# Performance work log

Hardware: AMD Instinct MI355X
Metric: run time of the kernel (lower is better)

## Reference

```python
import jax, jax.numpy as jnp
import numpy as np

N_NODES = 50000
N_EDGES = 300000
D = 256          # in_dim = out_dim (residual)
DE = 256         # edge relation dim
K = 2            # num_kgs
H = 4            # heads
L = 2            # layers
DH = D // H


def _routed_linear(x, W, b, idx):
    # x:[E,din], W:[K,din,dout], b:[K,dout], idx:[E] in [0,K)
    # Compute all K branches (K is tiny) then select per edge.
    outs = jnp.einsum('ed,kdo->keo', x, W) + b[:, None, :]
    return outs[idx, jnp.arange(idx.shape[0])]


def _layernorm(x, g, b):
    mu = jnp.mean(x, axis=-1, keepdims=True)
    var = jnp.mean(jnp.square(x - mu), axis=-1, keepdims=True)
    return (x - mu) * jax.lax.rsqrt(var + 1e-5) * g + b


def _mga_layer(h, src, dst, kg_src, kg_dst, beta, rel,
               ln_g, ln_b, Wt, bt, Wq, bq, Wk, bk):
    N = h.shape[0]
    E = src.shape[0]
    residual = h
    hn = _layernorm(h, ln_g, ln_b)
    x_j = hn[src]                       # [E,D] gathered source feats
    x_i = hn[dst]                       # [E,D] gathered target feats
    # per-edge KG-routed transfer of concatenated (x_j, relation emb)
    xj_t = jax.nn.gelu(_routed_linear(jnp.concatenate([x_j, rel], axis=1), Wt, bt, kg_src),
                       approximate=False)
    q = _routed_linear(x_i, Wq, bq, kg_dst).reshape(E, H, DH)
    k = _routed_linear(xj_t, Wk, bk, kg_src).reshape(E, H, DH)
    # per-edge multi-head dot product, scaled by edge_beta_r then 1/sqrt(dh)
    att = jnp.sum(q * k, axis=-1) * beta[:, None] / jnp.sqrt(jnp.asarray(DH, h.dtype))  # [E,H]
    # scatter-softmax over incoming edges of each target node
    m = jax.ops.segment_max(att, dst, num_segments=N)          # [N,H]
    e = jnp.exp(att - m[dst])
    denom = jax.ops.segment_sum(e, dst, num_segments=N)        # [N,H]
    a = e / (denom[dst] + 1e-16)                                # [E,H]
    msg = (a[:, :, None] * xj_t.reshape(E, H, DH)).reshape(E, D)
    aggr = jax.ops.segment_sum(msg, dst, num_segments=N)        # [N,D]
    return residual + jax.nn.gelu(aggr, approximate=False)


def setup_inputs() -> dict:
    key = jax.random.key(0)
    ks = jax.random.split(key, 10)
    x = jax.random.normal(ks[0], (N_NODES, D), dtype=jnp.float32)
    edge_index = jax.random.randint(ks[1], (2, N_EDGES), 0, N_NODES, dtype=jnp.int32)
    edge_kg_index = jax.random.randint(ks[2], (2, N_EDGES), 0, K, dtype=jnp.int32)
    edge_beta_r = jax.random.uniform(ks[3], (N_EDGES,), dtype=jnp.float32)
    edge_rel_emb = jax.random.normal(ks[4], (N_EDGES, DE), dtype=jnp.float32)
    return {
        'x': x,
        'edge_index': edge_index,
        'edge_kg_index': edge_kg_index,
        'edge_beta_r': edge_beta_r,
        'edge_rel_emb': edge_rel_emb,
        'ln_g': jnp.ones((L, D), jnp.float32),
        'ln_b': jnp.zeros((L, D), jnp.float32),
        'Wt': jax.random.normal(ks[5], (L, K, D + DE, D), jnp.float32) / np.sqrt(D + DE),
        'bt': jnp.zeros((L, K, D), jnp.float32),
        'Wq': jax.random.normal(ks[6], (L, K, D, D), jnp.float32) / np.sqrt(D),
        'bq': jnp.zeros((L, K, D), jnp.float32),
        'Wk': jax.random.normal(ks[7], (L, K, D, D), jnp.float32) / np.sqrt(D),
        'bk': jnp.zeros((L, K, D), jnp.float32),
    }


def reference(x, edge_index, edge_kg_index, edge_beta_r, edge_rel_emb,
              ln_g, ln_b, Wt, bt, Wq, bq, Wk, bk):
    src, dst = edge_index[0], edge_index[1]          # j (source), i (target)
    kg_src, kg_dst = edge_kg_index[0], edge_kg_index[1]
    h = x  # dropout is identity in eval mode
    for l in range(L):
        h = _mga_layer(h, src, dst, kg_src, kg_dst, edge_beta_r, edge_rel_emb,
                       ln_g[l], ln_b[l], Wt[l], bt[l], Wq[l], bq[l], Wk[l], bk[l])
    return h
```

## Files before the change

### kernel.cpp

```cpp
#include <hip/hip_runtime.h>
#include <hip/hip_bf16.h>

#define NN 50000
#define NE 300000
#define DD 256
#define NCHUNK 293

typedef __hip_bfloat16 bf16;
typedef __attribute__((ext_vector_type(8))) short bf16x8;
typedef __attribute__((ext_vector_type(4))) float f32x4;

__device__ __forceinline__ float bf2f(bf16 v) { return __bfloat162float(v); }
__device__ __forceinline__ unsigned short f2b(float v) {
    bf16 t = __float2bfloat16(v);
    return *reinterpret_cast<unsigned short*>(&t);
}
__device__ __forceinline__ float b2f_bits(unsigned short u) {
    return __uint_as_float(((unsigned)u) << 16);
}
__device__ __forceinline__ float gelu_f(float v) {
    float v2 = v * v;
    float z  = v * fmaf(v2, 0.044715f, 1.0f) * 0.7978845608f;
    float e  = __expf(2.0f * z);
    float th = 1.0f - 2.0f / (e + 1.0f);
    return 0.5f * v * (1.0f + th);
}
__device__ __forceinline__ void gl2lds16(const uint4* g, uint4* l) {
    __builtin_amdgcn_global_load_lds(
        (const __attribute__((address_space(1))) void*)g,
        (__attribute__((address_space(3))) void*)l, 16, 0, 0);
}

__global__ void part_count(const int* __restrict__ kg, int* __restrict__ bcnt) {
    int base = blockIdx.x * 1024;
    __shared__ int wc[4];
    int t = threadIdx.x, wave = t >> 6, lane = t & 63;
    int cnt = 0;
    #pragma unroll
    for (int s = 0; s < 4; ++s) {
        int j = base + s * 256 + t;
        int is0 = (j < NE && kg[j] == 0) ? 1 : 0;
        unsigned long long m = __ballot(is0);
        if (lane == 0) cnt += __popcll(m);
    }
    if (lane == 0) wc[wave] = cnt;
    __syncthreads();
    if (t == 0) bcnt[blockIdx.x] = wc[0] + wc[1] + wc[2] + wc[3];
}

__global__ void part_scan(const int* __restrict__ bcnt, int* __restrict__ bofs,
                          int* __restrict__ meta, int n) {
    if (threadIdx.x == 0 && blockIdx.x == 0) {
        int run = 0;
        for (int i = 0; i < n; ++i) { bofs[i] = run; run += bcnt[i]; }
        meta[0] = run;
    }
}

__global__ void part_scatter(const int* __restrict__ kg, const int* __restrict__ bofs,
                             const int* __restrict__ meta, int* __restrict__ perm) {
    int base = blockIdx.x * 1024;
    int c0 = meta[0];
    __shared__ int wz[4];
    int t = threadIdx.x, wave = t >> 6, lane = t & 63;
    int zrun = bofs[blockIdx.x];
    for (int s = 0; s < 4; ++s) {
        int j = base + s * 256 + t;
        int valid = j < NE;
        int is0 = (valid && kg[j] == 0) ? 1 : 0;
        unsigned long long m = __ballot(is0);
        int zb = __popcll(m & ((1ull << lane) - 1ull));
        if (lane == 0) wz[wave] = __popcll(m);
        __syncthreads();
        int wbefore = 0;
        for (int w = 0; w < wave; ++w) wbefore += wz[w];
        int zeros_before = zrun + wbefore + zb;
        if (valid) {
            int pos = is0 ? zeros_before : (c0 + (j - zeros_before));
            perm[pos] = j;
        }
        int stepz = wz[0] + wz[1] + wz[2] + wz[3];
        __syncthreads();
        zrun += stepz;
    }
}

__global__ void deg_hist(const int* __restrict__ dst, int* __restrict__ deg) {
    int i = blockIdx.x * blockDim.x + threadIdx.x;
    if (i < NE) atomicAdd(&deg[dst[i]], 1);
}

__global__ __launch_bounds__(1024) void scan_nodes(const int* __restrict__ deg,
                                                   int* __restrict__ ofs) {
    __shared__ int pex[1025];
    int t = threadIdx.x;
    const int C = (NN + 1023) / 1024;
    int base = t * C;
    int s = 0;
    for (int j = 0; j < C; ++j) { int idx = base + j; if (idx < NN) s += deg[idx]; }
    pex[t + 1] = s;
    __syncthreads();
    if (t == 0) {
        pex[0] = 0;
        for (int i = 1; i <= 1024; ++i) pex[i] += pex[i - 1];
    }
    __syncthreads();
    int run = pex[t];
    for (int j = 0; j < C; ++j) {
        int idx = base + j;
        if (idx < NN) { ofs[idx] = run; run += deg[idx]; }
    }
    if (t == 1023) ofs[NN] = pex[1024];
}

__global__ void copy_int(const int* __restrict__ a, int* __restrict__ b, int n) {
    int i = blockIdx.x * blockDim.x + threadIdx.x;
    if (i < n) b[i] = a[i];
}

__global__ void csr_fill(const int* __restrict__ dst, int* __restrict__ cur,
                         int* __restrict__ eid) {
    int i = blockIdx.x * blockDim.x + threadIdx.x;
    if (i < NE) {
        int p = atomicAdd(&cur[dst[i]], 1);
        eid[p] = i;
    }
}

__global__ void f2b_vec_kernel(const float* __restrict__ in, ushort* __restrict__ out, long n4) {
    long i0 = (long)blockIdx.x * blockDim.x + threadIdx.x;
    long stride = (long)gridDim.x * blockDim.x;
    for (long i = i0; i < n4; i += stride) {
        float4 v = ((const float4*)in)[i];
        ushort4 o;
        o.x = f2b(v.x); o.y = f2b(v.y); o.z = f2b(v.z); o.w = f2b(v.w);
        ((ushort4*)out)[i] = o;
    }
}

__global__ void transpose_w_kernel(const float* __restrict__ in, ushort* __restrict__ out,
                                   int shift, long total) {
    long i0 = (long)blockIdx.x * blockDim.x + threadIdx.x;
    long stride = (long)gridDim.x * blockDim.x;
    long dmask = ((long)1 << shift) - 1;
    for (long i = i0; i < total; i += stride) {
        long d = i & dmask;
        long rest = i >> shift;
        long o = rest & 255;
        long s = rest >> 8;
        out[i] = f2b(in[((s << shift) + d) * 256 + o]);
    }
}

__global__ void fill_kernel(float* __restrict__ p, float v, int n) {
    for (int i = blockIdx.x * blockDim.x + threadIdx.x; i < n; i += gridDim.x * blockDim.x)
        p[i] = v;
}

__global__ __launch_bounds__(256) void lnx_kernel(const float* __restrict__ x,
        const float* __restrict__ g, const float* __restrict__ b,
        float* __restrict__ h, bf16* __restrict__ hn) {
    int n = blockIdx.x * 4 + (threadIdx.x >> 6);
    if (n >= NN) return;
    int t = threadIdx.x & 63;
    float4 v = ((const float4*)(x + (size_t)n * DD))[t];
    ((float4*)(h + (size_t)n * DD))[t] = v;
    float s  = v.x + v.y + v.z + v.w;
    float s2 = v.x * v.x + v.y * v.y + v.z * v.z + v.w * v.w;
    #pragma unroll
    for (int off = 32; off; off >>= 1) {
        s  += __shfl_down(s, off);
        s2 += __shfl_down(s2, off);
    }
    s = __shfl(s, 0); s2 = __shfl(s2, 0);
    float mu  = s * (1.f / DD);
    float var = s2 * (1.f / DD) - mu * mu;
    float rs  = rsqrtf(var + 1e-5f);
    float vv[4] = {v.x, v.y, v.z, v.w};
    ushort4 pk;
    unsigned short* pku = (unsigned short*)&pk;
    #pragma unroll
    for (int j = 0; j < 4; ++j) {
        int c = t * 4 + j;
        pku[j] = f2b((vv[j] - mu) * rs * g[c] + b[c]);
    }
    ((ushort4*)(hn + (size_t)n * DD))[t] = pk;
}

__global__ __launch_bounds__(512) void qn_mfma(
        const bf16* __restrict__ hn, const ushort* __restrict__ WqT,
        const float* __restrict__ bq, ushort* __restrict__ qn) {
    __shared__ uint4 xh[64 * 32];
    __shared__ float bqs[2][256];
    int t = threadIdx.x;
    int n0 = blockIdx.x * 64;
    int wave = t >> 6, lane = t & 63;
    if (t < 256) { bqs[0][t] = bq[t]; bqs[1][t] = bq[256 + t]; }
    const uint4* hn4 = (const uint4*)hn;
    #pragma unroll
    for (int j = 0; j < 4; ++j) {
        int pr = wave * 4 + j;
        int r2 = pr * 2 + (lane >> 5);
        int node = n0 + r2; if (node >= NN) node = NN - 1;
        int s = lane & 31;
        gl2lds16(hn4 + (size_t)node * 32 + (s ^ (r2 & 7)), &xh[pr * 64]);
    }
    __syncthreads();
    int lr = lane & 15, lg = lane >> 4;
    f32x4 acc[2][2][4];
    #pragma unroll
    for (int b = 0; b < 2; ++b)
        #pragma unroll
        for (int m = 0; m < 2; ++m)
            #pragma unroll
            for (int n = 0; n < 4; ++n) acc[b][m][n] = (f32x4){0.f, 0.f, 0.f, 0.f};
    const char* xhb = (const char*)xh;
    const ushort* qr0 = WqT + (size_t)(wave * 32 + lr) * 256 + lg * 8;
    const ushort* qr1 = WqT + (size_t)(wave * 32 + 16 + lr) * 256 + lg * 8;
    #pragma unroll
    for (int kk = 0; kk < 8; ++kk) {
        bf16x8 a00 = *(const bf16x8*)(qr0 + kk * 32);
        bf16x8 a01 = *(const bf16x8*)(qr1 + kk * 32);
        bf16x8 a10 = *(const bf16x8*)(qr0 + 65536 + kk * 32);
        bf16x8 a11 = *(const bf16x8*)(qr1 + 65536 + kk * 32);
        bf16x8 bfr[4];
        #pragma unroll
        for (int n = 0; n < 4; ++n) {
            int r = n * 16 + lr;
            bfr[n] = *(const bf16x8*)(xhb + r * 512 + (((kk * 4 + lg) ^ (r & 7)) << 4));
        }
        #pragma unroll
        for (int n = 0; n < 4; ++n) {
            acc[0][0][n] = __builtin_amdgcn_mfma_f32_16x16x32_bf16(a00, bfr[n], acc[0][0][n], 0, 0, 0);
            acc[0][1][n] = __builtin_amdgcn_mfma_f32_16x16x32_bf16(a01, bfr[n], acc[0][1][n], 0, 0, 0);
            acc[1][0][n] = __builtin_amdgcn_mfma_f32_16x16x32_bf16(a10, bfr[n], acc[1][0][n], 0, 0, 0);
            acc[1][1][n] = __builtin_amdgcn_mfma_f32_16x16x32_bf16(a11, bfr[n], acc[1][1][n], 0, 0, 0);
        }
    }
    #pragma unroll
    for (int n = 0; n < 4; ++n) {
        int e = n * 16 + lr;
        int node = n0 + e;
        if (node < NN) {
            #pragma unroll
            for (int br = 0; br < 2; ++br)
                #pragma unroll
                for (int m = 0; m < 2; ++m) {
                    int ob = wave * 32 + m * 16 + lg * 4;
                    f32x4 a = acc[br][m][n];
                    ushort4 pk;
                    unsigned short* pu = (unsigned short*)&pk;
                    #pragma unroll
                    for (int r = 0; r < 4; ++r) pu[r] = f2b(a[r] + bqs[br][ob + r]);
                    *(ushort4*)(qn + ((size_t)br * NN + node) * 256 + ob) = pk;
                }
        }
    }
}

template<int RELB>
__global__ __launch_bounds__(512, 4) void transfer_mfma(
        const bf16* __restrict__ hn, const float* __restrict__ rel,
        const ushort* __restrict__ relb,
        const int* __restrict__ src, const int* __restrict__ dst,
        const int* __restrict__ kgd,
        const int* __restrict__ perm, const int* __restrict__ meta,
        const ushort* __restrict__ WtT, const float* __restrict__ bt,
        const ushort* __restrict__ WkT, const float* __restrict__ bk,
        const ushort* __restrict__ qn, const float* __restrict__ beta,
        bf16* __restrict__ xjt, float* __restrict__ att) {
    __shared__ uint4 xh[64 * 32];
    __shared__ float bts[256], bks[256];
    __shared__ float patt[8][64];
    __shared__ int sge[64], ssrc[64], sdst[64], sgd[64], sval[64];
    int t = threadIdx.x;
    int c0 = meta[0];
    int tiles0 = (c0 + 63) >> 6;
    int tiles1 = (NE - c0 + 63) >> 6;
    int bid = blockIdx.x;
    if (bid >= tiles0 + tiles1) return;
    int kgt, start, end;
    if (bid < tiles0) { kgt = 0; start = bid * 64; end = c0; }
    else              { kgt = 1; start = c0 + (bid - tiles0) * 64; end = NE; }
    int wave = t >> 6, lane = t & 63;
    if (t < 64) {
        int pos = start + t;
        int v = pos < end;
        int ge = perm[v ? pos : end - 1];
        sge[t] = ge; sval[t] = v; ssrc[t] = src[ge]; sdst[t] = dst[ge]; sgd[t] = kgd[ge];
    } else if (t >= 256) {
        int c = t & 255;
        bts[c] = bt[kgt * 256 + c];
        bks[c] = bk[kgt * 256 + c];
    }
    __syncthreads();
    const uint4* hn4 = (const uint4*)hn;
    #pragma unroll
    for (int j = 0; j < 4; ++j) {
        int pr = wave * 4 + j;
        int r2 = pr * 2 + (lane >> 5);
        int s = lane & 31;
        gl2lds16(hn4 + (size_t)ssrc[r2] * 32 + (s ^ (r2 & 7)), &xh[pr * 64]);
    }
    __syncthreads();
    int lr = lane & 15, lg = lane >> 4;
    ushort4 kv[2][4];
    #pragma unroll
    for (int n = 0; n < 4; ++n) {
        int e = n * 16 + lr;
        size_t qb = ((size_t)sgd[e] * NN + sdst[e]) * 256;
        #pragma unroll
        for (int m = 0; m < 2; ++m) {
            int ob = wave * 32 + m * 16 + lg * 4;
            kv[m][n] = *(const ushort4*)(qn + qb + ob);
        }
    }
    f32x4 acc[2][4];
    #pragma unroll
    for (int m = 0; m < 2; ++m)
        #pragma unroll
        for (int n = 0; n < 4; ++n) acc[m][n] = (f32x4){0.f, 0.f, 0.f, 0.f};
    const char* xhb = (const char*)xh;
    const ushort* wb = WtT + (size_t)kgt * 131072;
    const ushort* wrow0 = wb + (size_t)(wave * 32 + lr) * 512 + lg * 8;
    const ushort* wrow1 = wb + (size_t)(wave * 32 + 16 + lr) * 512 + lg * 8;
    __builtin_amdgcn_s_setprio(1);
    #pragma unroll
    for (int kk = 0; kk < 8; ++kk) {
        bf16x8 a0 = *(const bf16x8*)(wrow0 + kk * 32);
        bf16x8 a1 = *(const bf16x8*)(wrow1 + kk * 32);
        bf16x8 bfr[4];
        #pragma unroll
        for (int n = 0; n < 4; ++n) {
            int r = n * 16 + lr;
            bfr[n] = *(const bf16x8*)(xhb + r * 512 + (((kk * 4 + lg) ^ (r & 7)) << 4));
        }
        #pragma unroll
        for (int m = 0; m < 2; ++m)
            #pragma unroll
            for (int n = 0; n < 4; ++n)
                acc[m][n] = __builtin_amdgcn_mfma_f32_16x16x32_bf16((m ? a1 : a0), bfr[n], acc[m][n], 0, 0, 0);
    }
    __builtin_amdgcn_s_setprio(0);
    __syncthreads();
    if (RELB) {
        const uint4* rb4 = (const uint4*)relb;
        #pragma unroll
        for (int j = 0; j < 4; ++j) {
            int pr = wave * 4 + j;
            int r2 = pr * 2 + (lane >> 5);
            int s = lane & 31;
            gl2lds16(rb4 + (size_t)sge[r2] * 32 + (s ^ (r2 & 7)), &xh[pr * 64]);
        }
    } else {
        #pragma unroll
        for (int i = 0; i < 8; ++i) {
            int r = i * 8 + wave;
            float4 f = ((const float4*)(rel + (size_t)sge[r] * 256))[lane];
            ushort4 o;
            o.x = f2b(f.x); o.y = f2b(f.y); o.z = f2b(f.z); o.w = f2b(f.w);
            int s = lane >> 1;
            char* bp = (char*)&xh[r * 32] + (((s ^ (r & 7)) << 4) | ((lane & 1) << 3));
            *(ushort4*)bp = o;
        }
    }
    __syncthreads();
    __builtin_amdgcn_s_setprio(1);
    #pragma unroll
    for (int kk = 8; kk < 16; ++kk) {
        bf16x8 a0 = *(const bf16x8*)(wrow0 + kk * 32);
        bf16x8 a1 = *(const bf16x8*)(wrow1 + kk * 32);
        int ks = (kk & 7) * 4 + lg;
        bf16x8 bfr[4];
        #pragma unroll
        for (int n = 0; n < 4; ++n) {
            int r = n * 16 + lr;
            bfr[n] = *(const bf16x8*)(xhb + r * 512 + ((ks ^ (r & 7)) << 4));
        }
        #pragma unroll
        for (int m = 0; m < 2; ++m)
            #pragma unroll
            for (int n = 0; n < 4; ++n)
                acc[m][n] = __builtin_amdgcn_mfma_f32_16x16x32_bf16((m ? a1 : a0), bfr[n], acc[m][n], 0, 0, 0);
    }
    __builtin_amdgcn_s_setprio(0);
    __syncthreads();
    char* xob = (char*)xh;
    #pragma unroll
    for (int n = 0; n < 4; ++n) {
        int e = n * 16 + lr;
        #pragma unroll
        for (int m = 0; m < 2; ++m) {
            int ob = wave * 32 + m * 16 + lg * 4;
            f32x4 a = acc[m][n];
            ushort4 pk;
            unsigned short* pu = (unsigned short*)&pk;
            #pragma unroll
            for (int r = 0; r < 4; ++r)
                pu[r] = f2b(gelu_f(a[r] + bts[ob + r]));
            int bofs = ob * 2;
            int slot = ((bofs >> 4) ^ (e & 7));
            *(ushort4*)(xob + e * 512 + slot * 16 + (bofs & 15)) = pk;
        }
    }
    __syncthreads();
    #pragma unroll
    for (int m = 0; m < 2; ++m)
        #pragma unroll
        for (int n = 0; n < 4; ++n) acc[m][n] = (f32x4){0.f, 0.f, 0.f, 0.f};
    const ushort* kbw = WkT + (size_t)kgt * 65536;
    const ushort* kr0 = kbw + (size_t)(wave * 32 + lr) * 256 + lg * 8;
    const ushort* kr1 = kbw + (size_t)(wave * 32 + 16 + lr) * 256 + lg * 8;
    __builtin_amdgcn_s_setprio(1);
    #pragma unroll
    for (int kk = 0; kk < 8; ++kk) {
        bf16x8 a0 = *(const bf16x8*)(kr0 + kk * 32);
        bf16x8 a1 = *(const bf16x8*)(kr1 + kk * 32);
        bf16x8 bfr[4];
        #pragma unroll
        for (int n = 0; n < 4; ++n) {
            int r = n * 16 + lr;
            bfr[n] = *(const bf16x8*)(xob + r * 512 + (((kk * 4 + lg) ^ (r & 7)) << 4));
        }
        #pragma unroll
        for (int n = 0; n < 4; ++n) {
            acc[0][n] = __builtin_amdgcn_mfma_f32_16x16x32_bf16(a0, bfr[n], acc[0][n], 0, 0, 0);
            acc[1][n] = __builtin_amdgcn_mfma_f32_16x16x32_bf16(a1, bfr[n], acc[1][n], 0, 0, 0);
        }
    }
    __builtin_amdgcn_s_setprio(0);
    float p[4];
    #pragma unroll
    for (int n = 0; n < 4; ++n) {
        float s = 0.f;
        #pragma unroll
        for (int m = 0; m < 2; ++m) {
            int ob = wave * 32 + m * 16 + lg * 4;
            ushort4 qv = kv[m][n];
            f32x4 kcv = acc[m][n];
            s = fmaf(b2f_bits(qv.x), kcv[0] + bks[ob + 0], s);
            s = fmaf(b2f_bits(qv.y), kcv[1] + bks[ob + 1], s);
            s = fmaf(b2f_bits(qv.z), kcv[2] + bks[ob + 2], s);
            s = fmaf(b2f_bits(qv.w), kcv[3] + bks[ob + 3], s);
        }
        p[n] = s;
    }
    #pragma unroll
    for (int n = 0; n < 4; ++n) {
        p[n] += __shfl_xor(p[n], 16);
        p[n] += __shfl_xor(p[n], 32);
    }
    if (lane < 16) {
        #pragma unroll
        for (int n = 0; n < 4; ++n) patt[wave][n * 16 + lr] = p[n];
    }
    uint4* xjv = (uint4*)xjt;
    #pragma unroll
    for (int i = 0; i < 4; ++i) {
        int flat = i * 512 + t;
        int r = flat >> 5, c = flat & 31;
        if (sval[r])
            xjv[(size_t)sge[r] * 32 + c] = *(const uint4*)(xob + r * 512 + ((c ^ (r & 7)) << 4));
    }
    __syncthreads();
    if (t < 256) {
        int e = t & 63, h = t >> 6;
        if (sval[e]) {
            int ge = sge[e];
            att[(size_t)ge * 4 + h] = (patt[2 * h][e] + patt[2 * h + 1][e]) * beta[ge] * 0.125f;
        }
    }
}

template<int WRITE_HN>
__global__ __launch_bounds__(256) void aggregate_kernel(
        const float* __restrict__ att, const bf16* __restrict__ xjt,
        const int* __restrict__ eid, const int* __restrict__ ofs,
        float* __restrict__ h, const float* __restrict__ g, const float* __restrict__ b,
        bf16* __restrict__ hn) {
    int node = blockIdx.x * 4 + (threadIdx.x >> 6);
    if (node >= NN) return;
    int lane = threadIdx.x & 63;
    int hh = lane >> 4;
    int beg = ofs[node], end = ofs[node + 1];
    float m = -1e30f;
    for (int i = beg; i < end; ++i)
        m = fmaxf(m, att[(size_t)eid[i] * 4 + hh]);
    float den = 0.f;
    float a0 = 0.f, a1 = 0.f, a2 = 0.f, a3 = 0.f;
    for (int i = beg; i < end; ++i) {
        int e = eid[i];
        float wgt = __expf(att[(size_t)e * 4 + hh] - m);
        den += wgt;
        ushort4 v = *(const ushort4*)((const ushort*)xjt + (size_t)e * 256 + lane * 4);
        a0 = fmaf(wgt, b2f_bits(v.x), a0);
        a1 = fmaf(wgt, b2f_bits(v.y), a1);
        a2 = fmaf(wgt, b2f_bits(v.z), a2);
        a3 = fmaf(wgt, b2f_bits(v.w), a3);
    }
    float inv = 1.f / (den + 1e-16f);
    float4 hv = ((float4*)(h + (size_t)node * 256))[lane];
    hv.x += gelu_f(a0 * inv);
    hv.y += gelu_f(a1 * inv);
    hv.z += gelu_f(a2 * inv);
    hv.w += gelu_f(a3 * inv);
    ((float4*)(h + (size_t)node * 256))[lane] = hv;
    if (WRITE_HN) {
        float s  = hv.x + hv.y + hv.z + hv.w;
        float s2 = hv.x * hv.x + hv.y * hv.y + hv.z * hv.z + hv.w * hv.w;
        #pragma unroll
        for (int off = 32; off; off >>= 1) {
            s  += __shfl_down(s, off);
            s2 += __shfl_down(s2, off);
        }
        s = __shfl(s, 0); s2 = __shfl(s2, 0);
        float mu  = s * (1.f / DD);
        float var = s2 * (1.f / DD) - mu * mu;
        float rs  = rsqrtf(var + 1e-5f);
        float vv[4] = {hv.x, hv.y, hv.z, hv.w};
        ushort4 pk;
        unsigned short* pku = (unsigned short*)&pk;
        #pragma unroll
        for (int j = 0; j < 4; ++j) {
            int c = lane * 4 + j;
            pku[j] = f2b((vv[j] - mu) * rs * g[c] + b[c]);
        }
        ((ushort4*)(hn + (size_t)node * DD))[lane] = pk;
    }
}

extern "C" void kernel_launch(void* const* d_in, const int* in_sizes, int n_in,
                              void* d_out, int out_size, void* d_ws, size_t ws_size,
                              hipStream_t stream) {
    const float* x    = (const float*)d_in[0];
    const int*   ei   = (const int*)d_in[1];
    const int*   ekg  = (const int*)d_in[2];
    const float* beta = (const float*)d_in[3];
    const float* rel  = (const float*)d_in[4];
    const float* ln_g = (const float*)d_in[5];
    const float* ln_b = (const float*)d_in[6];
    const float* Wt   = (const float*)d_in[7];
    const float* bt   = (const float*)d_in[8];
    const float* Wq   = (const float*)d_in[9];
    const float* bq   = (const float*)d_in[10];
    const float* Wk   = (const float*)d_in[11];
    const float* bk   = (const float*)d_in[12];

    float* h = (float*)d_out;

    const int* srcp = ei;
    const int* dstp = ei + NE;
    const int* kgs  = ekg;
    const int* kgd  = ekg + NE;

    char* w = (char*)d_ws;
    float*  att   = (float*)w;  w += (size_t)NE * 4 * 4;
    bf16*   hn    = (bf16*)w;   w += (size_t)NN * DD * 2;
    bf16*   xjt   = (bf16*)w;   w += (size_t)NE * DD * 2;
    ushort* qn    = (ushort*)w; w += (size_t)2 * NN * DD * 2;
    ushort* WtT   = (ushort*)w; w += (size_t)4 * 256 * 512 * 2;
    ushort* WqT   = (ushort*)w; w += (size_t)4 * 256 * 256 * 2;
    ushort* WkT   = (ushort*)w; w += (size_t)4 * 256 * 256 * 2;
    int* perm_src = (int*)w;    w += (size_t)NE * 4;
    int* bcnt0    = (int*)w;    w += NCHUNK * 4;
    int* bofs0    = (int*)w;    w += NCHUNK * 4;
    int* meta0    = (int*)w;    w += 64;
    int* deg      = (int*)w;    w += (size_t)NN * 4;
    int* ofs      = (int*)w;    w += (size_t)(NN + 1) * 4;
    int* cur      = (int*)w;    w += (size_t)NN * 4;
    int* eid      = (int*)w;    w += (size_t)NE * 4;
    size_t used = (size_t)(w - (char*)d_ws);
    ushort* relb = (ushort*)w;
    int use_relb = (ws_size >= used + (size_t)NE * DD * 2) ? 1 : 0;

    part_count<<<NCHUNK, 256, 0, stream>>>(kgs, bcnt0);
    part_scan<<<1, 64, 0, stream>>>(bcnt0, bofs0, meta0, NCHUNK);
    part_scatter<<<NCHUNK, 256, 0, stream>>>(kgs, bofs0, meta0, perm_src);

    fill_kernel<<<64, 256, 0, stream>>>((float*)deg, 0.f, NN);
    deg_hist<<<(NE + 255) / 256, 256, 0, stream>>>(dstp, deg);
    scan_nodes<<<1, 1024, 0, stream>>>(deg, ofs);
    copy_int<<<(NN + 255) / 256, 256, 0, stream>>>(ofs, cur, NN);
    csr_fill<<<(NE + 255) / 256, 256, 0, stream>>>(dstp, cur, eid);

    if (use_relb)
        f2b_vec_kernel<<<2048, 256, 0, stream>>>(rel, relb, (long)NE * DD / 4);
    transpose_w_kernel<<<512, 256, 0, stream>>>(Wt, WtT, 9, (long)4 * 256 * 512);
    transpose_w_kernel<<<256, 256, 0, stream>>>(Wq, WqT, 8, (long)4 * 256 * 256);
    transpose_w_kernel<<<256, 256, 0, stream>>>(Wk, WkT, 8, (long)4 * 256 * 256);

    const int EBP = (NE + 126) / 64;
    const int QB  = (NN + 63) / 64;
    const int AGB = (NN + 3) / 4;

    lnx_kernel<<<AGB, 256, 0, stream>>>(x, ln_g, ln_b, h, hn);
    for (int l = 0; l < 2; ++l) {
        qn_mfma<<<QB, 512, 0, stream>>>(hn, WqT + (size_t)l * 2 * 256 * 256, bq + l * 512, qn);
        if (use_relb)
            transfer_mfma<1><<<EBP, 512, 0, stream>>>(hn, rel, relb, srcp, dstp, kgd,
                    perm_src, meta0,
                    WtT + (size_t)l * 2 * 256 * 512, bt + l * 512,
                    WkT + (size_t)l * 2 * 256 * 256, bk + l * 512, qn, beta, xjt, att);
        else
            transfer_mfma<0><<<EBP, 512, 0, stream>>>(hn, rel, relb, srcp, dstp, kgd,
                    perm_src, meta0,
                    WtT + (size_t)l * 2 * 256 * 512, bt + l * 512,
                    WkT + (size_t)l * 2 * 256 * 256, bk + l * 512, qn, beta, xjt, att);
        if (l == 0)
            aggregate_kernel<1><<<AGB, 256, 0, stream>>>(att, xjt, eid, ofs, h,
                    ln_g + DD, ln_b + DD, hn);
        else
            aggregate_kernel<0><<<AGB, 256, 0, stream>>>(att, xjt, eid, ofs, h,
                    ln_g, ln_b, hn);
    }
}
```

Baseline: 1.206 ms.

## Precompute per-node hn·Wt_top for both KGs and gather it per edge

The x_j half of the routed transfer linear is moved from per-edge (300k rows) to per-node (50k rows, both KG branches). The node kernel now computes hn·Wt[:256] plus bias into a new bf16 buffer, and the edge kernel gathers that buffer as the accumulator initialiser, then only multiplies the relation-embedding half. This cuts the edge MFMA work for that stage roughly in half but adds node-side GEMMs, an extra buffer, and rounding of the partial sum to bf16. The single-thread partition scan is also replaced by a 512-thread parallel scan.

```diff
diff --git a/kernel.cpp b/kernel.cpp
--- a/kernel.cpp
+++ b/kernel.cpp
@@ -48,13 +48,23 @@
     if (t == 0) bcnt[blockIdx.x] = wc[0] + wc[1] + wc[2] + wc[3];
 }
 
-__global__ void part_scan(const int* __restrict__ bcnt, int* __restrict__ bofs,
-                          int* __restrict__ meta, int n) {
-    if (threadIdx.x == 0 && blockIdx.x == 0) {
-        int run = 0;
-        for (int i = 0; i < n; ++i) { bofs[i] = run; run += bcnt[i]; }
-        meta[0] = run;
-    }
+__global__ __launch_bounds__(512) void part_scan(const int* __restrict__ bcnt,
+                                                 int* __restrict__ bofs,
+                                                 int* __restrict__ meta, int n) {
+    __shared__ int tmp[512];
+    int t = threadIdx.x;
+    int v = (t < n) ? bcnt[t] : 0;
+    tmp[t] = v;
+    __syncthreads();
+    #pragma unroll
+    for (int off = 1; off < 512; off <<= 1) {
+        int u = (t >= off) ? tmp[t - off] : 0;
+        __syncthreads();
+        tmp[t] += u;
+        __syncthreads();
+    }
+    if (t < n) bofs[t] = tmp[t] - v;
+    if (t == n - 1) meta[0] = tmp[t];
 }
 
 __global__ void part_scatter(const int* __restrict__ kg, const int* __restrict__ bofs,
@@ -187,15 +197,18 @@
     ((ushort4*)(hn + (size_t)n * DD))[t] = pk;
 }
 
-__global__ __launch_bounds__(512) void qn_mfma(
-        const bf16* __restrict__ hn, const ushort* __restrict__ WqT,
-        const float* __restrict__ bq, ushort* __restrict__ qn) {
+__global__ __launch_bounds__(512) void nodeq_mfma(
+        const bf16* __restrict__ hn,
+        const ushort* __restrict__ WqT, const float* __restrict__ bq,
+        const ushort* __restrict__ WtT, const float* __restrict__ bt,
+        ushort* __restrict__ qn, ushort* __restrict__ hw) {
     __shared__ uint4 xh[64 * 32];
-    __shared__ float bqs[2][256];
+    __shared__ float bqs[2][256], bts[2][256];
     int t = threadIdx.x;
     int n0 = blockIdx.x * 64;
     int wave = t >> 6, lane = t & 63;
     if (t < 256) { bqs[0][t] = bq[t]; bqs[1][t] = bq[256 + t]; }
+    else { int c = t & 255; bts[0][c] = bt[c]; bts[1][c] = bt[256 + c]; }
     const uint4* hn4 = (const uint4*)hn;
     #pragma unroll
     for (int j = 0; j < 4; ++j) {
@@ -207,6 +220,7 @@
     }
     __syncthreads();
     int lr = lane & 15, lg = lane >> 4;
+    const char* xhb = (const char*)xh;
     f32x4 acc[2][2][4];
     #pragma unroll
     for (int b = 0; b < 2; ++b)
@@ -214,27 +228,77 @@
         for (int m = 0; m < 2; ++m)
             #pragma unroll
             for (int n = 0; n < 4; ++n) acc[b][m][n] = (f32x4){0.f, 0.f, 0.f, 0.f};
-    const char* xhb = (const char*)xh;
-    const ushort* qr0 = WqT + (size_t)(wave * 32 + lr) * 256 + lg * 8;
-    const ushort* qr1 = WqT + (size_t)(wave * 32 + 16 + lr) * 256 + lg * 8;
-    #pragma unroll
-    for (int kk = 0; kk < 8; ++kk) {
-        bf16x8 a00 = *(const bf16x8*)(qr0 + kk * 32);
-        bf16x8 a01 = *(const bf16x8*)(qr1 + kk * 32);
-        bf16x8 a10 = *(const bf16x8*)(qr0 + 65536 + kk * 32);
-        bf16x8 a11 = *(const bf16x8*)(qr1 + 65536 + kk * 32);
-        bf16x8 bfr[4];
-        #pragma unroll
-        for (int n = 0; n < 4; ++n) {
-            int r = n * 16 + lr;
-            bfr[n] = *(const bf16x8*)(xhb + r * 512 + (((kk * 4 + lg) ^ (r & 7)) << 4));
-        }
-        #pragma unroll
-        for (int n = 0; n < 4; ++n) {
-            acc[0][0][n] = __builtin_amdgcn_mfma_f32_16x16x32_bf16(a00, bfr[n], acc[0][0][n], 0, 0, 0);
-            acc[0][1][n] = __builtin_amdgcn_mfma_f32_16x16x32_bf16(a01, bfr[n], acc[0][1][n], 0, 0, 0);
-            acc[1][0][n] = __builtin_amdgcn_mfma_f32_16x16x32_bf16(a10, bfr[n], acc[1][0][n], 0, 0, 0);
-            acc[1][1][n] = __builtin_amdgcn_mfma_f32_16x16x32_bf16(a11, bfr[n], acc[1][1][n], 0, 0, 0);
+    {
+        const ushort* tr0 = WtT + (size_t)(wave * 32 + lr) * 512 + lg * 8;
+        const ushort* tr1 = WtT + (size_t)(wave * 32 + 16 + lr) * 512 + lg * 8;
+        #pragma unroll
+        for (int kk = 0; kk < 8; ++kk) {
+            bf16x8 a00 = *(const bf16x8*)(tr0 + kk * 32);
+            bf16x8 a01 = *(const bf16x8*)(tr1 + kk * 32);
+            bf16x8 a10 = *(const bf16x8*)(tr0 + 131072 + kk * 32);
+            bf16x8 a11 = *(const bf16x8*)(tr1 + 131072 + kk * 32);
+            bf16x8 bfr[4];
+            #pragma unroll
+            for (int n = 0; n < 4; ++n) {
+                int r = n * 16 + lr;
+                bfr[n] = *(const bf16x8*)(xhb + r * 512 + (((kk * 4 + lg) ^ (r & 7)) << 4));
+            }
+            #pragma unroll
+            for (int n = 0; n < 4; ++n) {
+                acc[0][0][n] = __builtin_amdgcn_mfma_f32_16x16x32_bf16(a00, bfr[n], acc[0][0][n], 0, 0, 0);
+                acc[0][1][n] = __builtin_amdgcn_mfma_f32_16x16x32_bf16(a01, bfr[n], acc[0][1][n], 0, 0, 0);
+                acc[1][0][n] = __builtin_amdgcn_mfma_f32_16x16x32_bf16(a10, bfr[n], acc[1][0][n], 0, 0, 0);
+                acc[1][1][n] = __builtin_amdgcn_mfma_f32_16x16x32_bf16(a11, bfr[n], acc[1][1][n], 0, 0, 0);
+            }
+        }
+    }
+    #pragma unroll
+    for (int n = 0; n < 4; ++n) {
+        int e = n * 16 + lr;
+        int node = n0 + e;
+        if (node < NN) {
+            #pragma unroll
+            for (int br = 0; br < 2; ++br)
+                #pragma unroll
+                for (int m = 0; m < 2; ++m) {
+                    int ob = wave * 32 + m * 16 + lg * 4;
+                    f32x4 a = acc[br][m][n];
+                    ushort4 pk;
+                    unsigned short* pu = (unsigned short*)&pk;
+                    #pragma unroll
+                    for (int r = 0; r < 4; ++r) pu[r] = f2b(a[r] + bts[br][ob + r]);
+                    *(ushort4*)(hw + ((size_t)br * NN + node) * 256 + ob) = pk;
+                }
+        }
+    }
+    #pragma unroll
+    for (int b = 0; b < 2; ++b)
+        #pragma unroll
+        for (int m = 0; m < 2; ++m)
+            #pragma unroll
+            for (int n = 0; n < 4; ++n) acc[b][m][n] = (f32x4){0.f, 0.f, 0.f, 0.f};
+    {
+        const ushort* qr0 = WqT + (size_t)(wave * 32 + lr) * 256 + lg * 8;
+        const ushort* qr1 = WqT + (size_t)(wave * 32 + 16 + lr) * 256 + lg * 8;
+        #pragma unroll
+        for (int kk = 0; kk < 8; ++kk) {
+            bf16x8 a00 = *(const bf16x8*)(qr0 + kk * 32);
+            bf16x8 a01 = *(const bf16x8*)(qr1 + kk * 32);
+            bf16x8 a10 = *(const bf16x8*)(qr0 + 65536 + kk * 32);
+            bf16x8 a11 = *(const bf16x8*)(qr1 + 65536 + kk * 32);
+            bf16x8 bfr[4];
+            #pragma unroll
+            for (int n = 0; n < 4; ++n) {
+                int r = n * 16 + lr;
+                bfr[n] = *(const bf16x8*)(xhb + r * 512 + (((kk * 4 + lg) ^ (r & 7)) << 4));
+            }
+            #pragma unroll
+            for (int n = 0; n < 4; ++n) {
+                acc[0][0][n] = __builtin_amdgcn_mfma_f32_16x16x32_bf16(a00, bfr[n], acc[0][0][n], 0, 0, 0);
+                acc[0][1][n] = __builtin_amdgcn_mfma_f32_16x16x32_bf16(a01, bfr[n], acc[0][1][n], 0, 0, 0);
+                acc[1][0][n] = __builtin_amdgcn_mfma_f32_16x16x32_bf16(a10, bfr[n], acc[1][0][n], 0, 0, 0);
+                acc[1][1][n] = __builtin_amdgcn_mfma_f32_16x16x32_bf16(a11, bfr[n], acc[1][1][n], 0, 0, 0);
+            }
         }
     }
     #pragma unroll
@@ -260,17 +324,17 @@
 
 template<int RELB>
 __global__ __launch_bounds__(512, 4) void transfer_mfma(
-        const bf16* __restrict__ hn, const float* __restrict__ rel,
-        const ushort* __restrict__ relb,
+        const float* __restrict__ rel, const ushort* __restrict__ relb,
         const int* __restrict__ src, const int* __restrict__ dst,
         const int* __restrict__ kgd,
         const int* __restrict__ perm, const int* __restrict__ meta,
-        const ushort* __restrict__ WtT, const float* __restrict__ bt,
+        const ushort* __restrict__ WtT,
         const ushort* __restrict__ WkT, const float* __restrict__ bk,
-        const ushort* __restrict__ qn, const float* __restrict__ beta,
+        const ushort* __restrict__ qn, const ushort* __restrict__ hw,
+        const float* __restrict__ beta,
         bf16* __restrict__ xjt, float* __restrict__ att) {
-    __shared__ uint4 xh[64 * 32];
-    __shared__ float bts[256], bks[256];
+    __shared__ uint4 xr[64 * 32];
+    __shared__ float bks[256];
     __shared__ float patt[8][64];
     __shared__ int sge[64], ssrc[64], sdst[64], sgd[64], sval[64];
     int t = threadIdx.x;
@@ -289,59 +353,8 @@
         int ge = perm[v ? pos : end - 1];
         sge[t] = ge; sval[t] = v; ssrc[t] = src[ge]; sdst[t] = dst[ge]; sgd[t] = kgd[ge];
     } else if (t >= 256) {
-        int c = t & 255;
-        bts[c] = bt[kgt * 256 + c];
-        bks[c] = bk[kgt * 256 + c];
-    }
-    __syncthreads();
-    const uint4* hn4 = (const uint4*)hn;
-    #pragma unroll
-    for (int j = 0; j < 4; ++j) {
-        int pr = wave * 4 + j;
-        int r2 = pr * 2 + (lane >> 5);
-        int s = lane & 31;
-        gl2lds16(hn4 + (size_t)ssrc[r2] * 32 + (s ^ (r2 & 7)), &xh[pr * 64]);
-    }
-    __syncthreads();
-    int lr = lane & 15, lg = lane >> 4;
-    ushort4 kv[2][4];
-    #pragma unroll
-    for (int n = 0; n < 4; ++n) {
-        int e = n * 16 + lr;
-        size_t qb = ((size_t)sgd[e] * NN + sdst[e]) * 256;
-        #pragma unroll
-        for (int m = 0; m < 2; ++m) {
-            int ob = wave * 32 + m * 16 + lg * 4;
-            kv[m][n] = *(const ushort4*)(qn + qb + ob);
-        }
-    }
-    f32x4 acc[2][4];
-    #pragma unroll
-    for (int m = 0; m < 2; ++m)
-        #pragma unroll
-        for (int n = 0; n < 4; ++n) acc[m][n] = (f32x4){0.f, 0.f, 0.f, 0.f};
-    const char* xhb = (const char*)xh;
-    const ushort* wb = WtT + (size_t)kgt * 131072;
-    const ushort* wrow0 = wb + (size_t)(wave * 32 + lr) * 512 + lg * 8;
-    const ushort* wrow1 = wb + (size_t)(wave * 32 + 16 + lr) * 512 + lg * 8;
-    __builtin_amdgcn_s_setprio(1);
-    #pragma unroll
-    for (int kk = 0; kk < 8; ++kk) {
-        bf16x8 a0 = *(const bf16x8*)(wrow0 + kk * 32);
-        bf16x8 a1 = *(const bf16x8*)(wrow1 + kk * 32);
-        bf16x8 bfr[4];
-        #pragma unroll
-        for (int n = 0; n < 4; ++n) {
-            int r = n * 16 + lr;
-            bfr[n] = *(const bf16x8*)(xhb + r * 512 + (((kk * 4 + lg) ^ (r & 7)) << 4));
-        }
-        #pragma unroll
-        for (int m = 0; m < 2; ++m)
-            #pragma unroll
-            for (int n = 0; n < 4; ++n)
-                acc[m][n] = __builtin_amdgcn_mfma_f32_16x16x32_bf16((m ? a1 : a0), bfr[n], acc[m][n], 0, 0, 0);
-    }
-    __builtin_amdgcn_s_setprio(0);
+        bks[t - 256] = bk[kgt * 256 + (t - 256)];
+    }
     __syncthreads();
     if (RELB) {
         const uint4* rb4 = (const uint4*)relb;
@@ -350,7 +363,7 @@
             int pr = wave * 4 + j;
             int r2 = pr * 2 + (lane >> 5);
             int s = lane & 31;
-            gl2lds16(rb4 + (size_t)sge[r2] * 32 + (s ^ (r2 & 7)), &xh[pr * 64]);
+            gl2lds16(rb4 + (size_t)sge[r2] * 32 + (s ^ (r2 & 7)), &xr[pr * 64]);
         }
     } else {
         #pragma unroll
@@ -360,22 +373,47 @@
             ushort4 o;
             o.x = f2b(f.x); o.y = f2b(f.y); o.z = f2b(f.z); o.w = f2b(f.w);
             int s = lane >> 1;
-            char* bp = (char*)&xh[r * 32] + (((s ^ (r & 7)) << 4) | ((lane & 1) << 3));
+            char* bp = (char*)&xr[r * 32] + (((s ^ (r & 7)) << 4) | ((lane & 1) << 3));
             *(ushort4*)bp = o;
         }
     }
-    __syncthreads();
+    int lr = lane & 15, lg = lane >> 4;
+    ushort4 kv[2][4], iw[2][4];
+    #pragma unroll
+    for (int n = 0; n < 4; ++n) {
+        int e = n * 16 + lr;
+        size_t qb = ((size_t)sgd[e] * NN + sdst[e]) * 256;
+        size_t hb = ((size_t)kgt   * NN + ssrc[e]) * 256;
+        #pragma unroll
+        for (int m = 0; m < 2; ++m) {
+            int ob = wave * 32 + m * 16 + lg * 4;
+            kv[m][n] = *(const ushort4*)(qn + qb + ob);
+            iw[m][n] = *(const ushort4*)(hw + hb + ob);
+        }
+    }
+    __syncthreads();
+    f32x4 acc[2][4];
+    #pragma unroll
+    for (int m = 0; m < 2; ++m)
+        #pragma unroll
+        for (int n = 0; n < 4; ++n) {
+            ushort4 w4 = iw[m][n];
+            acc[m][n] = (f32x4){b2f_bits(w4.x), b2f_bits(w4.y), b2f_bits(w4.z), b2f_bits(w4.w)};
+        }
+    const char* xrb = (const char*)xr;
+    const ushort* wb = WtT + (size_t)kgt * 131072;
+    const ushort* wrow0 = wb + (size_t)(wave * 32 + lr) * 512 + 256 + lg * 8;
+    const ushort* wrow1 = wb + (size_t)(wave * 32 + 16 + lr) * 512 + 256 + lg * 8;
     __builtin_amdgcn_s_setprio(1);
     #pragma unroll
-    for (int kk = 8; kk < 16; ++kk) {
+    for (int kk = 0; kk < 8; ++kk) {
         bf16x8 a0 = *(const bf16x8*)(wrow0 + kk * 32);
         bf16x8 a1 = *(const bf16x8*)(wrow1 + kk * 32);
-        int ks = (kk & 7) * 4 + lg;
         bf16x8 bfr[4];
         #pragma unroll
         for (int n = 0; n < 4; ++n) {
             int r = n * 16 + lr;
-            bfr[n] = *(const bf16x8*)(xhb + r * 512 + ((ks ^ (r & 7)) << 4));
+            bfr[n] = *(const bf16x8*)(xrb + r * 512 + (((kk * 4 + lg) ^ (r & 7)) << 4));
         }
         #pragma unroll
         for (int m = 0; m < 2; ++m)
@@ -385,7 +423,7 @@
     }
     __builtin_amdgcn_s_setprio(0);
     __syncthreads();
-    char* xob = (char*)xh;
+    char* xob = (char*)xr;
     #pragma unroll
     for (int n = 0; n < 4; ++n) {
         int e = n * 16 + lr;
@@ -397,7 +435,7 @@
             unsigned short* pu = (unsigned short*)&pk;
             #pragma unroll
             for (int r = 0; r < 4; ++r)
-                pu[r] = f2b(gelu_f(a[r] + bts[ob + r]));
+                pu[r] = f2b(gelu_f(a[r]));
             int bofs = ob * 2;
             int slot = ((bofs >> 4) ^ (e & 7));
             *(ushort4*)(xob + e * 512 + slot * 16 + (bofs & 15)) = pk;
@@ -558,6 +596,7 @@
     bf16*   hn    = (bf16*)w;   w += (size_t)NN * DD * 2;
     bf16*   xjt   = (bf16*)w;   w += (size_t)NE * DD * 2;
     ushort* qn    = (ushort*)w; w += (size_t)2 * NN * DD * 2;
+    ushort* hw    = (ushort*)w; w += (size_t)2 * NN * DD * 2;
     ushort* WtT   = (ushort*)w; w += (size_t)4 * 256 * 512 * 2;
     ushort* WqT   = (ushort*)w; w += (size_t)4 * 256 * 256 * 2;
     ushort* WkT   = (ushort*)w; w += (size_t)4 * 256 * 256 * 2;
@@ -574,7 +613,7 @@
     int use_relb = (ws_size >= used + (size_t)NE * DD * 2) ? 1 : 0;
 
     part_count<<<NCHUNK, 256, 0, stream>>>(kgs, bcnt0);
-    part_scan<<<1, 64, 0, stream>>>(bcnt0, bofs0, meta0, NCHUNK);
+    part_scan<<<1, 512, 0, stream>>>(bcnt0, bofs0, meta0, NCHUNK);
     part_scatter<<<NCHUNK, 256, 0, stream>>>(kgs, bofs0, meta0, perm_src);
 
     fill_kernel<<<64, 256, 0, stream>>>((float*)deg, 0.f, NN);
@@ -595,17 +634,19 @@
 
     lnx_kernel<<<AGB, 256, 0, stream>>>(x, ln_g, ln_b, h, hn);
     for (int l = 0; l < 2; ++l) {
-        qn_mfma<<<QB, 512, 0, stream>>>(hn, WqT + (size_t)l * 2 * 256 * 256, bq + l * 512, qn);
+        nodeq_mfma<<<QB, 512, 0, stream>>>(hn,
+                WqT + (size_t)l * 2 * 256 * 256, bq + l * 512,
+                WtT + (size_t)l * 2 * 256 * 512, bt + l * 512, qn, hw);
         if (use_relb)
-            transfer_mfma<1><<<EBP, 512, 0, stream>>>(hn, rel, relb, srcp, dstp, kgd,
+            transfer_mfma<1><<<EBP, 512, 0, stream>>>(rel, relb, srcp, dstp, kgd,
                     perm_src, meta0,
-                    WtT + (size_t)l * 2 * 256 * 512, bt + l * 512,
-                    WkT + (size_t)l * 2 * 256 * 256, bk + l * 512, qn, beta, xjt, att);
+                    WtT + (size_t)l * 2 * 256 * 512,
+                    WkT + (size_t)l * 2 * 256 * 256, bk + l * 512, qn, hw, beta, xjt, att);
         else
-            transfer_mfma<0><<<EBP, 512, 0, stream>>>(hn, rel, relb, srcp, dstp, kgd,
+            transfer_mfma<0><<<EBP, 512, 0, stream>>>(rel, relb, srcp, dstp, kgd,
                     perm_src, meta0,
-                    WtT + (size_t)l * 2 * 256 * 512, bt + l * 512,
-                    WkT + (size_t)l * 2 * 256 * 256, bk + l * 512, qn, beta, xjt, att);
+                    WtT + (size_t)l * 2 * 256 * 512,
+                    WkT + (size_t)l * 2 * 256 * 256, bk + l * 512, qn, hw, beta, xjt, att);
         if (l == 0)
             aggregate_kernel<1><<<AGB, 256, 0, stream>>>(att, xjt, eid, ofs, h,
                     ln_g + DD, ln_b + DD, hn);
```

Result: no change. 1.194 ms (-1.0%).
